# Kernel tuning notes

Measured on AMD Instinct MI355X. Metric: run time of the kernel, lower is better.

Reference implementation:

```python
import math
import jax, jax.numpy as jnp
import numpy as np

B, S, G, CMAX, T = 128, 256, 8, 6, 32
E, NH, L, Z = 64, 4, 2, 3
DFF = 4 * E


def _conv1d(x, w, b, pad):
    # x: [N, C, T], w: [O, I, K] -> [N, O, T]
    y = jax.lax.conv_general_dilated(x, w, (1,), [(pad, pad)], dimension_numbers=('NCH', 'OIH', 'NCH'))
    return y + b[None, :, None]


def _layernorm(x, g, b, eps=1e-5):
    m = jnp.mean(x, -1, keepdims=True)
    v = jnp.mean((x - m) ** 2, -1, keepdims=True)
    return (x - m) * jax.lax.rsqrt(v + eps) * g + b


def _pos_encoding(seq_len, dim):
    pos = jnp.arange(seq_len, dtype=jnp.float32)[:, None]
    div = jnp.exp(jnp.arange(0, dim, 2, dtype=jnp.float32) * (-math.log(10000.0) / dim))
    pe = jnp.zeros((seq_len, dim), dtype=jnp.float32)
    pe = pe.at[:, 0::2].set(jnp.sin(pos * div)).at[:, 1::2].set(jnp.cos(pos * div))
    return pe


def setup_inputs() -> dict:
    key = jax.random.key(0)
    ks = iter(jax.random.split(key, 48))
    def nrm(shape, s=0.05):
        return (jax.random.normal(next(ks), shape) * s).astype(jnp.float32)
    inp = {}
    inp['waveforms'] = jax.random.normal(next(ks), (B, S, CMAX, T), dtype=jnp.float32)
    inp['shank_ids'] = jax.random.randint(next(ks), (B, S), 0, G)
    lengths = jax.random.randint(next(ks), (B,), S // 2, S + 1)
    inp['mask'] = jnp.arange(S)[None, :] >= lengths[:, None]  # True = padded
    inp['conv1_w'] = nrm((G, 32, CMAX, 5), 0.1)
    inp['conv1_b'] = jnp.zeros((G, 32), jnp.float32)
    inp['conv2_w'] = nrm((G, E, 32, 3), 0.1)
    inp['conv2_b'] = jnp.zeros((G, E), jnp.float32)
    inp['shank_emb'] = nrm((G, E), 0.02)
    inp['in_proj_w'] = nrm((L, 3 * E, E))
    inp['in_proj_b'] = jnp.zeros((L, 3 * E), jnp.float32)
    inp['out_proj_w'] = nrm((L, E, E))
    inp['out_proj_b'] = jnp.zeros((L, E), jnp.float32)
    inp['ln1_g'] = jnp.ones((L, E), jnp.float32)
    inp['ln1_b'] = jnp.zeros((L, E), jnp.float32)
    inp['ff1_w'] = nrm((L, DFF, E))
    inp['ff1_b'] = jnp.zeros((L, DFF), jnp.float32)
    inp['ff2_w'] = nrm((L, E, DFF))
    inp['ff2_b'] = jnp.zeros((L, E), jnp.float32)
    inp['ln2_g'] = jnp.ones((L, E), jnp.float32)
    inp['ln2_b'] = jnp.zeros((L, E), jnp.float32)
    inp['cls_w1'] = nrm((E, E)); inp['cls_b1'] = jnp.zeros((E,), jnp.float32)
    inp['cls_w2'] = nrm((Z, E)); inp['cls_b2'] = jnp.zeros((Z,), jnp.float32)
    inp['mu_w1'] = nrm((Z, E, E)); inp['mu_b1'] = jnp.zeros((Z, E), jnp.float32)
    inp['mu_w2'] = nrm((Z, 2, E)); inp['mu_b2'] = jnp.zeros((Z, 2), jnp.float32)
    inp['ls_w1'] = nrm((Z, E, E)); inp['ls_b1'] = jnp.zeros((Z, E), jnp.float32)
    inp['ls_w2'] = nrm((Z, 2, E)); inp['ls_b2'] = jnp.zeros((Z, 2), jnp.float32)
    inp['d_w1'] = nrm((E, E)); inp['d_b1'] = jnp.zeros((E,), jnp.float32)
    inp['d_w2'] = nrm((1, E)); inp['d_b2'] = jnp.zeros((1,), jnp.float32)
    return inp


def reference(waveforms, shank_ids, mask, conv1_w, conv1_b, conv2_w, conv2_b, shank_emb,
              in_proj_w, in_proj_b, out_proj_w, out_proj_b, ln1_g, ln1_b,
              ff1_w, ff1_b, ff2_w, ff2_b, ln2_g, ln2_b,
              cls_w1, cls_b1, cls_w2, cls_b2, mu_w1, mu_b1, mu_w2, mu_b2,
              ls_w1, ls_b1, ls_w2, ls_b2, d_w1, d_b1, d_w2, d_b2):
    b, s, c, t = waveforms.shape
    e = shank_emb.shape[1]
    g = shank_emb.shape[0]
    x = waveforms.reshape(b * s, c, t)
    # per-shank conv encoders (MoE-style dispatch); loop over fixed small expert set
    embs = []
    for i in range(g):
        h1 = jax.nn.relu(_conv1d(x, conv1_w[i], conv1_b[i], 2))   # [N,32,T]
        h2 = jax.nn.relu(_conv1d(h1, conv2_w[i], conv2_b[i], 1))  # [N,E,T]
        embs.append(h2.mean(-1))                                  # AdaptiveAvgPool1d(1)
    emb_all = jnp.stack(embs, axis=1)                             # [N,G,E]
    sid = shank_ids.reshape(-1)
    emb = jnp.take_along_axis(emb_all, sid[:, None, None], axis=1)[:, 0]  # [N,E]
    active = (~mask).reshape(-1)
    emb = jnp.where(active[:, None], emb, 0.0).reshape(b, s, e)   # masked slots stay zero
    emb = emb + shank_emb[shank_ids] + _pos_encoding(s, e)[None]
    # post-norm transformer encoder, relu FFN, eval mode (dropout off)
    dh = e // NH
    key_bias = jnp.where(mask, -1e9, 0.0).astype(emb.dtype)[:, None, None, :]  # [B,1,1,S]
    h = emb
    for l in range(in_proj_w.shape[0]):
        qkv = h @ in_proj_w[l].T + in_proj_b[l]
        q, k, v = jnp.split(qkv, 3, axis=-1)
        q = q.reshape(b, s, NH, dh)
        k = k.reshape(b, s, NH, dh)
        v = v.reshape(b, s, NH, dh)
        scores = jnp.einsum('bqhd,bkhd->bhqk', q, k) / math.sqrt(dh) + key_bias
        attn = jax.nn.softmax(scores, axis=-1)
        o = jnp.einsum('bhqk,bkhd->bqhd', attn, v).reshape(b, s, e)
        o = o @ out_proj_w[l].T + out_proj_b[l]
        h = _layernorm(h + o, ln1_g[l], ln1_b[l])
        ff = jax.nn.relu(h @ ff1_w[l].T + ff1_b[l]) @ ff2_w[l].T + ff2_b[l]
        h = _layernorm(h + ff, ln2_g[l], ln2_b[l])
    am = active.reshape(b, s, 1).astype(h.dtype)
    pooled = (h * am).sum(1) / (am.sum(1) + 1e-8)                 # masked mean pool [B,E]
    cls_logits = jax.nn.relu(pooled @ cls_w1.T + cls_b1) @ cls_w2.T + cls_b2
    hz = jax.nn.relu(jnp.einsum('be,zfe->zbf', pooled, mu_w1) + mu_b1[:, None])
    mus = jnp.einsum('zbf,zof->bzo', hz, mu_w2) + mu_b2[None]     # [B,Z,2]
    hs = jax.nn.relu(jnp.einsum('be,zfe->zbf', pooled, ls_w1) + ls_b1[:, None])
    sigmas = jnp.exp(jnp.einsum('zbf,zof->bzo', hs, ls_w2) + ls_b2[None])  # [B,Z,2]
    d_pred = jax.nn.sigmoid(jax.nn.relu(pooled @ d_w1.T + d_b1) @ d_w2.T + d_b2)
    return jnp.concatenate([cls_logits, mus.reshape(b, -1), sigmas.reshape(b, -1), d_pred], axis=-1)
```

## Files before the change

kernel.cpp:

```cpp
#include <hip/hip_runtime.h>
#include <math.h>


typedef short bf16x8 __attribute__((ext_vector_type(8)));
typedef float f32x4 __attribute__((ext_vector_type(4)));

__device__ __forceinline__ unsigned short f2bf(float f) {
  unsigned u = __float_as_uint(f);
  u += 0x7fffu + ((u >> 16) & 1u);
  return (unsigned short)(u >> 16);
}

__device__ __forceinline__ bf16x8 ldfrag(const unsigned short* p) {
  return *reinterpret_cast<const bf16x8*>(p);
}

__device__ __forceinline__ void ld4(const float* p, float* dst) {
  float4 t = *reinterpret_cast<const float4*>(p);
  dst[0] = t.x; dst[1] = t.y; dst[2] = t.z; dst[3] = t.w;
}

__device__ __forceinline__ bool is_masked(const void* mask_, int flag, int idx) {
  return flag ? (((const unsigned char*)mask_)[idx] != 0)
              : (((const int*)mask_)[idx] != 0);
}

__global__ void detect_mask_kernel(const unsigned int* __restrict__ mw,
                                   int* __restrict__ flag, int* __restrict__ counts,
                                   int* __restrict__ lens) {
  __shared__ int sh;
  if (threadIdx.x == 0) sh = 0;
  __syncthreads();
  int bad = 0;
  for (int i = threadIdx.x; i < 8192; i += 256)
    if (mw[i] > 1u) bad = 1;
  if (bad) atomicOr(&sh, 1);
  if (threadIdx.x < 8) counts[threadIdx.x] = 0;
  if (threadIdx.x < 128) lens[threadIdx.x] = 0;
  __syncthreads();
  if (threadIdx.x == 0) *flag = sh;
}

__global__ __launch_bounds__(256) void bin_kernel(
    const int* __restrict__ sid, const void* __restrict__ mask_,
    const int* __restrict__ flagp, int* __restrict__ counts,
    int* __restrict__ lens, int* __restrict__ idxbuf) {
  __shared__ int lcnt[8];
  __shared__ int lbase[8];
  int b = blockIdx.x, tid = threadIdx.x;
  int n = b * 256 + tid;
  int flag = *flagp;
  bool act = !is_masked(mask_, flag, n);
  int g = act ? sid[n] : 0;
  if (tid < 8) lcnt[tid] = 0;
  __syncthreads();
  int pos = 0;
  if (act) pos = atomicAdd(&lcnt[g], 1);
  __syncthreads();
  if (tid < 8) lbase[tid] = atomicAdd(&counts[tid], lcnt[tid]);
  if (tid == 0)
    lens[b] = lcnt[0] + lcnt[1] + lcnt[2] + lcnt[3] +
              lcnt[4] + lcnt[5] + lcnt[6] + lcnt[7];
  __syncthreads();
  if (act) idxbuf[g * 32768 + lbase[g] + pos] = n;
}

__global__ __launch_bounds__(256) void init_emb_kernel(
    const int* __restrict__ sid, const float* __restrict__ shank_emb,
    float* __restrict__ hout) {
  int i = blockIdx.x * 256 + threadIdx.x;
  int n = i >> 6, e = i & 63, s = n & 255;
  int g = sid[n];
  float div = __expf(-(float)(e & ~1) * (9.21034037f / 64.f));
  float angle = (float)s * div;
  float pe = (e & 1) ? cosf(angle) : sinf(angle);
  hout[i] = shank_emb[g * 64 + e] + pe;
}

#define CONV_BPG 64
__global__ __launch_bounds__(256) void conv_mfma_kernel(
    const int* __restrict__ idxbuf, const int* __restrict__ counts,
    const float* __restrict__ wav,
    const float* __restrict__ w1_, const float* __restrict__ b1_,
    const float* __restrict__ w2_, const float* __restrict__ b2_,
    float* __restrict__ hout) {
  __shared__ __align__(16) unsigned short w1f[5][32][8];
  __shared__ __align__(16) unsigned short w2f[3][64][40];
  __shared__ float b1s[32];
  __shared__ float b2s[64];
  __shared__ __align__(16) unsigned short xT[8][36][8];
  __shared__ __align__(16) unsigned short h1T[8][34][40];
  int g = blockIdx.x & 7, bib = blockIdx.x >> 3;
  int tid = threadIdx.x;
  int wv = tid >> 6, lane = tid & 63, quad = lane >> 4, l15 = lane & 15;
  for (int i = tid; i < 1280; i += 256) {
    int k = i >> 8, rest = i & 255, oc = rest >> 3, ic = rest & 7;
    w1f[k][oc][ic] = (ic < 6) ? f2bf(w1_[g * 960 + oc * 30 + ic * 5 + k]) : 0;
  }
  for (int i = tid; i < 7680; i += 256) {
    int k = i / 2560, rest = i % 2560, e = rest / 40, ic = rest % 40;
    w2f[k][e][ic] = (ic < 32) ? f2bf(w2_[g * 6144 + e * 96 + ic * 3 + k]) : 0;
  }
  if (tid < 32) b1s[tid] = b1_[g * 32 + tid];
  if (tid < 64) b2s[tid] = b2_[g * 64 + tid];
  {
    unsigned int* xz = (unsigned int*)&xT[0][0][0];
    for (int i = tid; i < 1152; i += 256) xz[i] = 0;
  }
  for (int i = tid; i < 640; i += 256) {
    int tok = i / 80, rest = i % 80;
    h1T[tok][(rest >= 40) ? 33 : 0][rest % 40] = 0;
  }
  __syncthreads();
  bf16x8 zf = {0, 0, 0, 0, 0, 0, 0, 0};
  bf16x8 bf1[2], bf1k4[2], bf2[3][4];
#pragma unroll
  for (int nt = 0; nt < 2; nt++) {
    bf1[nt] = ldfrag(&w1f[quad][nt * 16 + l15][0]);
    bf1k4[nt] = (quad == 0) ? ldfrag(&w1f[4][nt * 16 + l15][0]) : zf;
  }
#pragma unroll
  for (int k = 0; k < 3; k++)
#pragma unroll
    for (int nt = 0; nt < 4; nt++)
      bf2[k][nt] = ldfrag(&w2f[k][nt * 16 + l15][quad * 8]);
  float b1v0 = b1s[l15], b1v1 = b1s[16 + l15];
  int cnt = counts[g];
  for (int base = bib * 8; base < cnt; base += CONV_BPG * 8) {
    __syncthreads();
    for (int i = tid; i < 384; i += 256) {
      int tok = i / 48, rem = i % 48, ic = rem >> 3, tq = rem & 7;
      int ti = base + tok;
      float4 v = make_float4(0.f, 0.f, 0.f, 0.f);
      if (ti < cnt)
        v = *(const float4*)&wav[idxbuf[g * 32768 + ti] * 192 + ic * 32 + tq * 4];
      int r0 = tq * 4 + 2;
      xT[tok][r0 + 0][ic] = f2bf(v.x);
      xT[tok][r0 + 1][ic] = f2bf(v.y);
      xT[tok][r0 + 2][ic] = f2bf(v.z);
      xT[tok][r0 + 3][ic] = f2bf(v.w);
    }
    __syncthreads();
#pragma unroll
    for (int ts = 0; ts < 2; ts++) {
      int tk = wv * 2 + ts;
      f32x4 c1[2][2];
#pragma unroll
      for (int mt = 0; mt < 2; mt++) {
        c1[mt][0] = (f32x4){b1v0, b1v0, b1v0, b1v0};
        c1[mt][1] = (f32x4){b1v1, b1v1, b1v1, b1v1};
      }
#pragma unroll
      for (int mt = 0; mt < 2; mt++) {
        bf16x8 afm = ldfrag(&xT[tk][mt * 16 + l15 + quad][0]);
        bf16x8 af4 = (quad == 0) ? ldfrag(&xT[tk][mt * 16 + l15 + 4][0]) : zf;
#pragma unroll
        for (int nt = 0; nt < 2; nt++) {
          c1[mt][nt] = __builtin_amdgcn_mfma_f32_16x16x32_bf16(afm, bf1[nt], c1[mt][nt], 0, 0, 0);
          c1[mt][nt] = __builtin_amdgcn_mfma_f32_16x16x32_bf16(af4, bf1k4[nt], c1[mt][nt], 0, 0, 0);
        }
      }
#pragma unroll
      for (int mt = 0; mt < 2; mt++)
#pragma unroll
        for (int nt = 0; nt < 2; nt++)
#pragma unroll
          for (int r = 0; r < 4; r++) {
            int t = mt * 16 + quad * 4 + r;
            h1T[tk][t + 1][nt * 16 + l15] = f2bf(fmaxf(c1[mt][nt][r], 0.f));
          }
    }
    __syncthreads();
#pragma unroll
    for (int ts = 0; ts < 2; ts++) {
      int tk = wv * 2 + ts;
      f32x4 c2[2][4];
#pragma unroll
      for (int mt = 0; mt < 2; mt++)
#pragma unroll
        for (int nt = 0; nt < 4; nt++) {
          float bv = b2s[nt * 16 + l15];
          c2[mt][nt] = (f32x4){bv, bv, bv, bv};
        }
#pragma unroll
      for (int k = 0; k < 3; k++)
#pragma unroll
        for (int mt = 0; mt < 2; mt++) {
          bf16x8 af = ldfrag(&h1T[tk][mt * 16 + l15 + k][quad * 8]);
#pragma unroll
          for (int nt = 0; nt < 4; nt++)
            c2[mt][nt] = __builtin_amdgcn_mfma_f32_16x16x32_bf16(af, bf2[k][nt], c2[mt][nt], 0, 0, 0);
        }
      int ti = base + tk;
      float sums[4];
#pragma unroll
      for (int nt = 0; nt < 4; nt++) {
        float s = 0.f;
#pragma unroll
        for (int mt = 0; mt < 2; mt++)
#pragma unroll
          for (int r = 0; r < 4; r++) s += fmaxf(c2[mt][nt][r], 0.f);
        s += __shfl_xor(s, 16);
        s += __shfl_xor(s, 32);
        sums[nt] = s;
      }
      if (ti < cnt && quad == 0) {
        int n = idxbuf[g * 32768 + ti];
#pragma unroll
        for (int nt = 0; nt < 4; nt++)
          hout[n * 64 + nt * 16 + l15] += sums[nt] * (1.f / 32.f);
      }
    }
  }
}

template <int NT, int MODE>
__global__ __launch_bounds__(256) void gemm_nt(
    const float* __restrict__ A, const float* __restrict__ W,
    const float* __restrict__ bias, float* __restrict__ C,
    float* __restrict__ H, const float* __restrict__ lng,
    const float* __restrict__ lnb, int K) {
  constexpr int N = NT * 16;
  __shared__ __align__(16) unsigned short As[64][72];
  __shared__ __align__(16) unsigned short Bs[N][72];
  int m0 = blockIdx.x * 64;
  int tid = threadIdx.x;
  int wv = tid >> 6, lane = tid & 63, quad = lane >> 4, l15 = lane & 15;
  f32x4 acc[NT];
#pragma unroll
  for (int nt = 0; nt < NT; nt++) {
    float b = bias[nt * 16 + l15];
    acc[nt] = (f32x4){b, b, b, b};
  }
  for (int kc = 0; kc < K; kc += 64) {
    __syncthreads();
    for (int i = tid; i < 1024; i += 256) {
      int r = i >> 4, c4 = (i & 15) << 2;
      float4 av = *(const float4*)&A[(size_t)(m0 + r) * K + kc + c4];
      short4 t;
      t.x = (short)f2bf(av.x); t.y = (short)f2bf(av.y);
      t.z = (short)f2bf(av.z); t.w = (short)f2bf(av.w);
      *(short4*)&As[r][c4] = t;
    }
    for (int i = tid; i < N * 16; i += 256) {
      int r = i >> 4, c4 = (i & 15) << 2;
      float4 wv4 = *(const float4*)&W[(size_t)r * K + kc + c4];
      short4 u;
      u.x = (short)f2bf(wv4.x); u.y = (short)f2bf(wv4.y);
      u.z = (short)f2bf(wv4.z); u.w = (short)f2bf(wv4.w);
      *(short4*)&Bs[r][c4] = u;
    }
    __syncthreads();
#pragma unroll
    for (int ks = 0; ks < 64; ks += 32) {
      bf16x8 af = ldfrag(&As[wv * 16 + l15][ks + quad * 8]);
#pragma unroll
      for (int nt = 0; nt < NT; nt++) {
        bf16x8 bfr = ldfrag(&Bs[nt * 16 + l15][ks + quad * 8]);
        acc[nt] = __builtin_amdgcn_mfma_f32_16x16x32_bf16(af, bfr, acc[nt], 0, 0, 0);
      }
    }
  }
  int mrow = m0 + wv * 16 + quad * 4;
  if (MODE <= 1) {
#pragma unroll
    for (int nt = 0; nt < NT; nt++)
#pragma unroll
      for (int r = 0; r < 4; r++) {
        float v = acc[nt][r];
        if (MODE == 1) v = fmaxf(v, 0.f);
        C[(size_t)(mrow + r) * N + nt * 16 + l15] = v;
      }
  } else {
#pragma unroll
    for (int r = 0; r < 4; r++) {
      float rv[4];
      float s = 0.f;
#pragma unroll
      for (int nt = 0; nt < 4; nt++) {
        float v = acc[nt][r] + H[(size_t)(mrow + r) * 64 + nt * 16 + l15];
        rv[nt] = v; s += v;
      }
      s += __shfl_xor(s, 1); s += __shfl_xor(s, 2);
      s += __shfl_xor(s, 4); s += __shfl_xor(s, 8);
      float mean = s * (1.f / 64.f);
      float vsum = 0.f;
#pragma unroll
      for (int nt = 0; nt < 4; nt++) { rv[nt] -= mean; vsum += rv[nt] * rv[nt]; }
      vsum += __shfl_xor(vsum, 1); vsum += __shfl_xor(vsum, 2);
      vsum += __shfl_xor(vsum, 4); vsum += __shfl_xor(vsum, 8);
      float inv = rsqrtf(vsum * (1.f / 64.f) + 1e-5f);
#pragma unroll
      for (int nt = 0; nt < 4; nt++) {
        int col = nt * 16 + l15;
        H[(size_t)(mrow + r) * 64 + col] = rv[nt] * inv * lng[col] + lnb[col];
      }
    }
  }
}

__global__ __launch_bounds__(256) void attn_kernel(
    const float* __restrict__ qkv, const int* __restrict__ lens,
    float* __restrict__ o) {
  __shared__ __align__(16) unsigned short qs[256][24];
  __shared__ __align__(16) unsigned short kst[256][24];
  __shared__ __align__(16) unsigned short vT[16][264];
  __shared__ __align__(16) unsigned short pw[4][16][264];
  int bh = blockIdx.x;
  int b_ = bh >> 2, hd = bh & 3;
  int tid = threadIdx.x;
  int wv = tid >> 6, lane = tid & 63, quad = lane >> 4, l15 = lane & 15;
  int len = lens[b_];
  const float* base = qkv + b_ * 256 * 192 + hd * 16;
  for (int i = tid; i < 1024; i += 256) {
    int s = i >> 2, c = (i & 3) << 2;
    const float* rp = base + s * 192;
    float4 q4 = *(const float4*)(rp + c);
    float4 k4 = *(const float4*)(rp + 64 + c);
    float4 v4 = *(const float4*)(rp + 128 + c);
    short4 qp, kp;
    qp.x = (short)f2bf(q4.x * 0.25f); qp.y = (short)f2bf(q4.y * 0.25f);
    qp.z = (short)f2bf(q4.z * 0.25f); qp.w = (short)f2bf(q4.w * 0.25f);
    kp.x = (short)f2bf(k4.x); kp.y = (short)f2bf(k4.y);
    kp.z = (short)f2bf(k4.z); kp.w = (short)f2bf(k4.w);
    *(short4*)&qs[s][c] = qp;
    *(short4*)&kst[s][c] = kp;
    vT[c + 0][s] = f2bf(v4.x);
    vT[c + 1][s] = f2bf(v4.y);
    vT[c + 2][s] = f2bf(v4.z);
    vT[c + 3][s] = f2bf(v4.w);
  }
  __syncthreads();
  bf16x8 zf = {0, 0, 0, 0, 0, 0, 0, 0};
  f32x4 zero = {0.f, 0.f, 0.f, 0.f};
#pragma unroll 1
  for (int j = 0; j < 4; j++) {
    int qt = wv * 4 + j;
    bf16x8 bq = (quad < 2) ? ldfrag(&qs[qt * 16 + l15][quad * 8]) : zf;
    f32x4 s[16];
#pragma unroll
    for (int t = 0; t < 16; t++) {
      bf16x8 ak = (quad < 2) ? ldfrag(&kst[t * 16 + l15][quad * 8]) : zf;
      s[t] = __builtin_amdgcn_mfma_f32_16x16x32_bf16(ak, bq, zero, 0, 0, 0);
    }
    float mx = -1e30f;
#pragma unroll
    for (int t = 0; t < 16; t++)
#pragma unroll
      for (int r = 0; r < 4; r++) {
        int key = t * 16 + quad * 4 + r;
        float v = (key < len) ? s[t][r] : -1e30f;
        s[t][r] = v;
        mx = fmaxf(mx, v);
      }
    mx = fmaxf(mx, __shfl_xor(mx, 16));
    mx = fmaxf(mx, __shfl_xor(mx, 32));
    float sum = 0.f;
#pragma unroll
    for (int t = 0; t < 16; t++)
#pragma unroll
      for (int r = 0; r < 4; r++) {
        float p = __expf(s[t][r] - mx);
        s[t][r] = p;
        sum += p;
      }
    sum += __shfl_xor(sum, 16);
    sum += __shfl_xor(sum, 32);
#pragma unroll
    for (int t = 0; t < 16; t++) {
      short4 pp;
      pp.x = (short)f2bf(s[t][0]); pp.y = (short)f2bf(s[t][1]);
      pp.z = (short)f2bf(s[t][2]); pp.w = (short)f2bf(s[t][3]);
      *(short4*)&pw[wv][l15][t * 16 + quad * 4] = pp;
    }
    f32x4 acc = zero;
#pragma unroll
    for (int c = 0; c < 8; c++) {
      bf16x8 av = ldfrag(&vT[l15][c * 32 + quad * 8]);
      bf16x8 bp = ldfrag(&pw[wv][l15][c * 32 + quad * 8]);
      acc = __builtin_amdgcn_mfma_f32_16x16x32_bf16(av, bp, acc, 0, 0, 0);
    }
    float inv = 1.f / sum;
    float4 w;
    w.x = acc[0] * inv; w.y = acc[1] * inv;
    w.z = acc[2] * inv; w.w = acc[3] * inv;
    *(float4*)&o[(size_t)(b_ * 256 + qt * 16 + l15) * 64 + hd * 16 + quad * 4] = w;
  }
}

__global__ __launch_bounds__(256) void pool_kernel(
    const float* __restrict__ h, const int* __restrict__ lens,
    float* __restrict__ pooled) {
  __shared__ float ps[4][64];
  int b = blockIdx.x;
  int e = threadIdx.x & 63, sp = threadIdx.x >> 6;
  int len = lens[b];
  float sum = 0.f;
  int send = min(sp * 64 + 64, len);
  for (int s = sp * 64; s < send; s++) sum += h[(b * 256 + s) * 64 + e];
  ps[sp][e] = sum;
  __syncthreads();
  if (sp == 0) {
    float tot = ps[0][e] + ps[1][e] + ps[2][e] + ps[3][e];
    pooled[b * 64 + e] = tot / ((float)len + 1e-8f);
  }
}

__global__ __launch_bounds__(64) void heads_kernel(
    const float* __restrict__ pooled,
    const float* __restrict__ cls_w1, const float* __restrict__ cls_b1,
    const float* __restrict__ cls_w2, const float* __restrict__ cls_b2,
    const float* __restrict__ mu_w1, const float* __restrict__ mu_b1,
    const float* __restrict__ mu_w2, const float* __restrict__ mu_b2,
    const float* __restrict__ ls_w1, const float* __restrict__ ls_b1,
    const float* __restrict__ ls_w2, const float* __restrict__ ls_b2,
    const float* __restrict__ d_w1, const float* __restrict__ d_b1,
    const float* __restrict__ d_w2, const float* __restrict__ d_b2,
    float* __restrict__ out) {
  int b = blockIdx.x, e = threadIdx.x;
  __shared__ float p[64];
  __shared__ float t1[64];
  p[e] = pooled[b * 64 + e];
  __syncthreads();
  {
    float a = cls_b1[e];
    for (int j = 0; j < 64; j++) a += p[j] * cls_w1[e * 64 + j];
    t1[e] = fmaxf(a, 0.f);
  }
  __syncthreads();
  if (e < 3) {
    float a2 = cls_b2[e];
    for (int j = 0; j < 64; j++) a2 += t1[j] * cls_w2[e * 64 + j];
    out[b * 16 + e] = a2;
  }
  for (int z = 0; z < 3; z++) {
    __syncthreads();
    {
      float a = mu_b1[z * 64 + e];
      for (int j = 0; j < 64; j++) a += p[j] * mu_w1[(z * 64 + e) * 64 + j];
      t1[e] = fmaxf(a, 0.f);
    }
    __syncthreads();
    if (e < 2) {
      float a2 = mu_b2[z * 2 + e];
      for (int j = 0; j < 64; j++) a2 += t1[j] * mu_w2[(z * 2 + e) * 64 + j];
      out[b * 16 + 3 + z * 2 + e] = a2;
    }
    __syncthreads();
    {
      float a = ls_b1[z * 64 + e];
      for (int j = 0; j < 64; j++) a += p[j] * ls_w1[(z * 64 + e) * 64 + j];
      t1[e] = fmaxf(a, 0.f);
    }
    __syncthreads();
    if (e < 2) {
      float a2 = ls_b2[z * 2 + e];
      for (int j = 0; j < 64; j++) a2 += t1[j] * ls_w2[(z * 2 + e) * 64 + j];
      out[b * 16 + 9 + z * 2 + e] = __expf(a2);
    }
  }
  __syncthreads();
  {
    float a = d_b1[e];
    for (int j = 0; j < 64; j++) a += p[j] * d_w1[e * 64 + j];
    t1[e] = fmaxf(a, 0.f);
  }
  __syncthreads();
  if (e == 0) {
    float a2 = d_b2[0];
    for (int j = 0; j < 64; j++) a2 += t1[j] * d_w2[j];
    out[b * 16 + 15] = 1.f / (1.f + __expf(-a2));
  }
}

extern "C" void kernel_launch(void* const* d_in, const int* in_sizes, int n_in,
                              void* d_out, int out_size, void* d_ws, size_t ws_size,
                              hipStream_t stream) {
  const float* wav       = (const float*)d_in[0];
  const int*   sid       = (const int*)d_in[1];
  const void*  mask      = d_in[2];
  const float* conv1_w   = (const float*)d_in[3];
  const float* conv1_b   = (const float*)d_in[4];
  const float* conv2_w   = (const float*)d_in[5];
  const float* conv2_b   = (const float*)d_in[6];
  const float* shank_emb = (const float*)d_in[7];
  const float* in_proj_w = (const float*)d_in[8];
  const float* in_proj_b = (const float*)d_in[9];
  const float* out_proj_w= (const float*)d_in[10];
  const float* out_proj_b= (const float*)d_in[11];
  const float* ln1_g     = (const float*)d_in[12];
  const float* ln1_b     = (const float*)d_in[13];
  const float* ff1_w     = (const float*)d_in[14];
  const float* ff1_b     = (const float*)d_in[15];
  const float* ff2_w     = (const float*)d_in[16];
  const float* ff2_b     = (const float*)d_in[17];
  const float* ln2_g     = (const float*)d_in[18];
  const float* ln2_b     = (const float*)d_in[19];
  const float* cls_w1    = (const float*)d_in[20];
  const float* cls_b1    = (const float*)d_in[21];
  const float* cls_w2    = (const float*)d_in[22];
  const float* cls_b2    = (const float*)d_in[23];
  const float* mu_w1     = (const float*)d_in[24];
  const float* mu_b1     = (const float*)d_in[25];
  const float* mu_w2     = (const float*)d_in[26];
  const float* mu_b2     = (const float*)d_in[27];
  const float* ls_w1     = (const float*)d_in[28];
  const float* ls_b1     = (const float*)d_in[29];
  const float* ls_w2     = (const float*)d_in[30];
  const float* ls_b2     = (const float*)d_in[31];
  const float* d_w1      = (const float*)d_in[32];
  const float* d_b1      = (const float*)d_in[33];
  const float* d_w2      = (const float*)d_in[34];
  const float* d_b2      = (const float*)d_in[35];
  float* out = (float*)d_out;

  float* ws = (float*)d_ws;
  float* h      = ws;
  float* qkv    = ws + 2097152;
  float* obuf   = ws + 8388608;
  float* ff     = ws + 2097152;
  float* pooled = ws + 10485760;
  int*   ip     = (int*)(ws + 10493952);
  int*   flag   = ip;
  int*   counts = ip + 8;
  int*   lens   = ip + 16;
  int*   idxbuf = ip + 144;

  detect_mask_kernel<<<1, 256, 0, stream>>>((const unsigned int*)mask, flag, counts, lens);
  bin_kernel<<<128, 256, 0, stream>>>(sid, mask, flag, counts, lens, idxbuf);
  init_emb_kernel<<<8192, 256, 0, stream>>>(sid, shank_emb, h);
  conv_mfma_kernel<<<CONV_BPG * 8, 256, 0, stream>>>(idxbuf, counts, wav, conv1_w, conv1_b,
                                                     conv2_w, conv2_b, h);
  for (int l = 0; l < 2; l++) {
    gemm_nt<12, 0><<<512, 256, 0, stream>>>(
        h, in_proj_w + l * 12288, in_proj_b + l * 192, qkv, nullptr, nullptr, nullptr, 64);
    attn_kernel<<<512, 256, 0, stream>>>(qkv, lens, obuf);
    gemm_nt<4, 2><<<512, 256, 0, stream>>>(
        obuf, out_proj_w + l * 4096, out_proj_b + l * 64, nullptr, h,
        ln1_g + l * 64, ln1_b + l * 64, 64);
    gemm_nt<16, 1><<<512, 256, 0, stream>>>(
        h, ff1_w + l * 16384, ff1_b + l * 256, ff, nullptr, nullptr, nullptr, 64);
    gemm_nt<4, 2><<<512, 256, 0, stream>>>(
        ff, ff2_w + l * 16384, ff2_b + l * 64, nullptr, h,
        ln2_g + l * 64, ln2_b + l * 64, 256);
  }
  pool_kernel<<<128, 256, 0, stream>>>(h, lens, pooled);
  heads_kernel<<<128, 64, 0, stream>>>(pooled, cls_w1, cls_b1, cls_w2, cls_b2,
                                       mu_w1, mu_b1, mu_w2, mu_b2,
                                       ls_w1, ls_b1, ls_w2, ls_b2,
                                       d_w1, d_b1, d_w2, d_b2, out);
}
```

Measured before the change: 373.3 us.

## Process one token per wavefront in conv kernel and fuse embedding add

```diff
diff --git a/kernel.cpp b/kernel.cpp
--- a/kernel.cpp
+++ b/kernel.cpp
@@ -77,19 +77,18 @@
   hout[i] = shank_emb[g * 64 + e] + pe;
 }
 
-#define CONV_BPG 64
 __global__ __launch_bounds__(256) void conv_mfma_kernel(
     const int* __restrict__ idxbuf, const int* __restrict__ counts,
     const float* __restrict__ wav,
     const float* __restrict__ w1_, const float* __restrict__ b1_,
     const float* __restrict__ w2_, const float* __restrict__ b2_,
-    float* __restrict__ hout) {
+    const float* __restrict__ shank_emb, float* __restrict__ hout) {
   __shared__ __align__(16) unsigned short w1f[5][32][8];
   __shared__ __align__(16) unsigned short w2f[3][64][40];
   __shared__ float b1s[32];
   __shared__ float b2s[64];
-  __shared__ __align__(16) unsigned short xT[8][36][8];
-  __shared__ __align__(16) unsigned short h1T[8][34][40];
+  __shared__ __align__(16) unsigned short xw[4][36][8];
+  __shared__ __align__(16) unsigned short h1w[4][34][40];
   int g = blockIdx.x & 7, bib = blockIdx.x >> 3;
   int tid = threadIdx.x;
   int wv = tid >> 6, lane = tid & 63, quad = lane >> 4, l15 = lane & 15;
@@ -104,12 +103,12 @@
   if (tid < 32) b1s[tid] = b1_[g * 32 + tid];
   if (tid < 64) b2s[tid] = b2_[g * 64 + tid];
   {
-    unsigned int* xz = (unsigned int*)&xT[0][0][0];
-    for (int i = tid; i < 1152; i += 256) xz[i] = 0;
-  }
-  for (int i = tid; i < 640; i += 256) {
-    int tok = i / 80, rest = i % 80;
-    h1T[tok][(rest >= 40) ? 33 : 0][rest % 40] = 0;
+    unsigned int* xz = (unsigned int*)&xw[wv][0][0];
+    for (int i = lane; i < 144; i += 64) xz[i] = 0;
+    unsigned int* hz0 = (unsigned int*)&h1w[wv][0][0];
+    unsigned int* hz1 = (unsigned int*)&h1w[wv][33][0];
+    if (lane < 20) hz0[lane] = 0;
+    else if (lane < 40) hz1[lane - 20] = 0;
   }
   __syncthreads();
   bf16x8 zf = {0, 0, 0, 0, 0, 0, 0, 0};
@@ -125,92 +124,83 @@
     for (int nt = 0; nt < 4; nt++)
       bf2[k][nt] = ldfrag(&w2f[k][nt * 16 + l15][quad * 8]);
   float b1v0 = b1s[l15], b1v1 = b1s[16 + l15];
+  float shank = shank_emb[g * 64 + lane];
+  float dive = __expf(-(float)(lane & ~1) * (9.21034037f / 64.f));
   int cnt = counts[g];
-  for (int base = bib * 8; base < cnt; base += CONV_BPG * 8) {
-    __syncthreads();
-    for (int i = tid; i < 384; i += 256) {
-      int tok = i / 48, rem = i % 48, ic = rem >> 3, tq = rem & 7;
-      int ti = base + tok;
-      float4 v = make_float4(0.f, 0.f, 0.f, 0.f);
-      if (ti < cnt)
-        v = *(const float4*)&wav[idxbuf[g * 32768 + ti] * 192 + ic * 32 + tq * 4];
-      int r0 = tq * 4 + 2;
-      xT[tok][r0 + 0][ic] = f2bf(v.x);
-      xT[tok][r0 + 1][ic] = f2bf(v.y);
-      xT[tok][r0 + 2][ic] = f2bf(v.z);
-      xT[tok][r0 + 3][ic] = f2bf(v.w);
-    }
-    __syncthreads();
-#pragma unroll
-    for (int ts = 0; ts < 2; ts++) {
-      int tk = wv * 2 + ts;
-      f32x4 c1[2][2];
+  int wvg = bib * 4 + wv;
+  int ic_w = lane >> 3, t0_w = (lane & 7) * 4;
+  for (int ti = wvg; ti < cnt; ti += 256) {
+    int n = idxbuf[g * 32768 + ti];
+    float4 v = make_float4(0.f, 0.f, 0.f, 0.f);
+    if (lane < 48) v = *(const float4*)&wav[n * 192 + lane * 4];
+    if (lane < 48) {
+      xw[wv][t0_w + 2][ic_w] = f2bf(v.x);
+      xw[wv][t0_w + 3][ic_w] = f2bf(v.y);
+      xw[wv][t0_w + 4][ic_w] = f2bf(v.z);
+      xw[wv][t0_w + 5][ic_w] = f2bf(v.w);
+    }
+    f32x4 c1[2][2];
+#pragma unroll
+    for (int mt = 0; mt < 2; mt++) {
+      c1[mt][0] = (f32x4){b1v0, b1v0, b1v0, b1v0};
+      c1[mt][1] = (f32x4){b1v1, b1v1, b1v1, b1v1};
+    }
+#pragma unroll
+    for (int mt = 0; mt < 2; mt++) {
+      bf16x8 afm = ldfrag(&xw[wv][mt * 16 + l15 + quad][0]);
+      bf16x8 af4 = (quad == 0) ? ldfrag(&xw[wv][mt * 16 + l15 + 4][0]) : zf;
+#pragma unroll
+      for (int nt = 0; nt < 2; nt++) {
+        c1[mt][nt] = __builtin_amdgcn_mfma_f32_16x16x32_bf16(afm, bf1[nt], c1[mt][nt], 0, 0, 0);
+        c1[mt][nt] = __builtin_amdgcn_mfma_f32_16x16x32_bf16(af4, bf1k4[nt], c1[mt][nt], 0, 0, 0);
+      }
+    }
+#pragma unroll
+    for (int mt = 0; mt < 2; mt++)
+#pragma unroll
+      for (int nt = 0; nt < 2; nt++)
+#pragma unroll
+        for (int r = 0; r < 4; r++) {
+          int t = mt * 16 + quad * 4 + r;
+          h1w[wv][t + 1][nt * 16 + l15] = f2bf(fmaxf(c1[mt][nt][r], 0.f));
+        }
+    f32x4 c2[2][4];
+#pragma unroll
+    for (int mt = 0; mt < 2; mt++)
+#pragma unroll
+      for (int nt = 0; nt < 4; nt++) {
+        float bv = b2s[nt * 16 + l15];
+        c2[mt][nt] = (f32x4){bv, bv, bv, bv};
+      }
+#pragma unroll
+    for (int k = 0; k < 3; k++)
 #pragma unroll
       for (int mt = 0; mt < 2; mt++) {
-        c1[mt][0] = (f32x4){b1v0, b1v0, b1v0, b1v0};
-        c1[mt][1] = (f32x4){b1v1, b1v1, b1v1, b1v1};
-      }
-#pragma unroll
-      for (int mt = 0; mt < 2; mt++) {
-        bf16x8 afm = ldfrag(&xT[tk][mt * 16 + l15 + quad][0]);
-        bf16x8 af4 = (quad == 0) ? ldfrag(&xT[tk][mt * 16 + l15 + 4][0]) : zf;
-#pragma unroll
-        for (int nt = 0; nt < 2; nt++) {
-          c1[mt][nt] = __builtin_amdgcn_mfma_f32_16x16x32_bf16(afm, bf1[nt], c1[mt][nt], 0, 0, 0);
-          c1[mt][nt] = __builtin_amdgcn_mfma_f32_16x16x32_bf16(af4, bf1k4[nt], c1[mt][nt], 0, 0, 0);
-        }
-      }
+        bf16x8 af = ldfrag(&h1w[wv][mt * 16 + l15 + k][quad * 8]);
+#pragma unroll
+        for (int nt = 0; nt < 4; nt++)
+          c2[mt][nt] = __builtin_amdgcn_mfma_f32_16x16x32_bf16(af, bf2[k][nt], c2[mt][nt], 0, 0, 0);
+      }
+    float sums[4];
+#pragma unroll
+    for (int nt = 0; nt < 4; nt++) {
+      float s = 0.f;
 #pragma unroll
       for (int mt = 0; mt < 2; mt++)
 #pragma unroll
-        for (int nt = 0; nt < 2; nt++)
-#pragma unroll
-          for (int r = 0; r < 4; r++) {
-            int t = mt * 16 + quad * 4 + r;
-            h1T[tk][t + 1][nt * 16 + l15] = f2bf(fmaxf(c1[mt][nt][r], 0.f));
-          }
-    }
-    __syncthreads();
-#pragma unroll
-    for (int ts = 0; ts < 2; ts++) {
-      int tk = wv * 2 + ts;
-      f32x4 c2[2][4];
-#pragma unroll
-      for (int mt = 0; mt < 2; mt++)
-#pragma unroll
-        for (int nt = 0; nt < 4; nt++) {
-          float bv = b2s[nt * 16 + l15];
-          c2[mt][nt] = (f32x4){bv, bv, bv, bv};
-        }
-#pragma unroll
-      for (int k = 0; k < 3; k++)
-#pragma unroll
-        for (int mt = 0; mt < 2; mt++) {
-          bf16x8 af = ldfrag(&h1T[tk][mt * 16 + l15 + k][quad * 8]);
-#pragma unroll
-          for (int nt = 0; nt < 4; nt++)
-            c2[mt][nt] = __builtin_amdgcn_mfma_f32_16x16x32_bf16(af, bf2[k][nt], c2[mt][nt], 0, 0, 0);
-        }
-      int ti = base + tk;
-      float sums[4];
-#pragma unroll
-      for (int nt = 0; nt < 4; nt++) {
-        float s = 0.f;
-#pragma unroll
-        for (int mt = 0; mt < 2; mt++)
-#pragma unroll
-          for (int r = 0; r < 4; r++) s += fmaxf(c2[mt][nt][r], 0.f);
-        s += __shfl_xor(s, 16);
-        s += __shfl_xor(s, 32);
-        sums[nt] = s;
-      }
-      if (ti < cnt && quad == 0) {
-        int n = idxbuf[g * 32768 + ti];
-#pragma unroll
-        for (int nt = 0; nt < 4; nt++)
-          hout[n * 64 + nt * 16 + l15] += sums[nt] * (1.f / 32.f);
-      }
-    }
+        for (int r = 0; r < 4; r++) s += fmaxf(c2[mt][nt][r], 0.f);
+      s += __shfl_xor(s, 16);
+      s += __shfl_xor(s, 32);
+      sums[nt] = s;
+    }
+    float t0 = __shfl(sums[0], l15);
+    float t1 = __shfl(sums[1], l15);
+    float t2 = __shfl(sums[2], l15);
+    float t3 = __shfl(sums[3], l15);
+    float val = (quad == 0) ? t0 : (quad == 1) ? t1 : (quad == 2) ? t2 : t3;
+    float angle = (float)(n & 255) * dive;
+    float pe = (lane & 1) ? cosf(angle) : sinf(angle);
+    hout[(size_t)n * 64 + lane] = val * (1.f / 32.f) + shank + pe;
   }
 }
 
@@ -529,8 +519,8 @@
   detect_mask_kernel<<<1, 256, 0, stream>>>((const unsigned int*)mask, flag, counts, lens);
   bin_kernel<<<128, 256, 0, stream>>>(sid, mask, flag, counts, lens, idxbuf);
   init_emb_kernel<<<8192, 256, 0, stream>>>(sid, shank_emb, h);
-  conv_mfma_kernel<<<CONV_BPG * 8, 256, 0, stream>>>(idxbuf, counts, wav, conv1_w, conv1_b,
-                                                     conv2_w, conv2_b, h);
+  conv_mfma_kernel<<<512, 256, 0, stream>>>(idxbuf, counts, wav, conv1_w, conv1_b,
+                                            conv2_w, conv2_b, shank_emb, h);
   for (int l = 0; l < 2; l++) {
     gemm_nt<12, 0><<<512, 256, 0, stream>>>(
         h, in_proj_w + l * 12288, in_proj_b + l * 192, qkv, nullptr, nullptr, nullptr, 64);
```

New measurement: 368.2 us. Within noise of the previous version (-1.4%).
